# Kernel tuning notes

Measured on AMD Instinct MI355X. Metric: run time of the kernel, lower is better.

## Reference

```python
import jax, jax.numpy as jnp
import numpy as np

EMBED_DIM = 1024
Q_IN = 1024
KV_IN = 256
NUM_HEADS = 16
HEAD_DIM = EMBED_DIM // NUM_HEADS
SCALING = HEAD_DIM ** -0.5
BSZ, TGT, SRC = 8, 1024, 1024


def setup_inputs() -> dict:
    key = jax.random.key(0)
    ks = jax.random.split(key, 12)
    s = lambda fan_in: 1.0 / np.sqrt(fan_in)
    return {
        "hidden_states": jax.random.normal(ks[0], (BSZ, TGT, Q_IN), jnp.float32),
        "key_value_states": jax.random.normal(ks[1], (BSZ, SRC, KV_IN), jnp.float32),
        "attention_mask": jnp.zeros((BSZ, 1, TGT, SRC), jnp.float32),
        "layer_head_mask": jnp.ones((NUM_HEADS,), jnp.float32),
        "Wq": jax.random.normal(ks[2], (Q_IN, EMBED_DIM), jnp.float32) * s(Q_IN),
        "bq": jax.random.normal(ks[3], (EMBED_DIM,), jnp.float32) * 0.02,
        "Wk": jax.random.normal(ks[4], (KV_IN, EMBED_DIM), jnp.float32) * s(KV_IN),
        "bk": jax.random.normal(ks[5], (EMBED_DIM,), jnp.float32) * 0.02,
        "Wv": jax.random.normal(ks[6], (KV_IN, EMBED_DIM), jnp.float32) * s(KV_IN),
        "bv": jax.random.normal(ks[7], (EMBED_DIM,), jnp.float32) * 0.02,
        "Wo": jax.random.normal(ks[8], (EMBED_DIM, EMBED_DIM), jnp.float32) * s(EMBED_DIM),
        "bo": jax.random.normal(ks[9], (EMBED_DIM,), jnp.float32) * 0.02,
    }


def reference(hidden_states, key_value_states, attention_mask, layer_head_mask,
              Wq, bq, Wk, bk, Wv, bv, Wo, bo):
    b, t, _ = hidden_states.shape
    src = key_value_states.shape[1]
    # projections, split heads: [b, h, len, d]
    q = (hidden_states @ Wq + bq) * SCALING
    q = q.reshape(b, t, NUM_HEADS, HEAD_DIM).transpose(0, 2, 1, 3)
    k = (key_value_states @ Wk + bk).reshape(b, src, NUM_HEADS, HEAD_DIM).transpose(0, 2, 1, 3)
    v = (key_value_states @ Wv + bv).reshape(b, src, NUM_HEADS, HEAD_DIM).transpose(0, 2, 1, 3)
    # scores [b, h, t, src] + additive mask
    scores = jnp.einsum("bhtd,bhsd->bhts", q, k) + attention_mask
    probs = jax.nn.softmax(scores, axis=-1)
    # head mask multiply (dropout p=0 in eval)
    probs = probs * layer_head_mask[None, :, None, None]
    out = jnp.einsum("bhts,bhsd->bhtd", probs, v)
    out = out.transpose(0, 2, 1, 3).reshape(b, t, EMBED_DIM)
    return out @ Wo + bo
```

## Files before the change

### kernel.cpp

```cpp
#include <hip/hip_runtime.h>
#include <hip/hip_bf16.h>
#include <cstdint>

#define B_    8
#define T_    1024
#define S_    1024
#define E_    1024
#define NH_   16
#define HD_   64
#define KVIN_ 256
#define SCALE_ 0.125f

typedef __attribute__((ext_vector_type(8))) short bf16x8;
typedef __attribute__((ext_vector_type(4))) float f32x4;
typedef unsigned short us;

__device__ __forceinline__ us f2bf(float x) {
  union { float f; unsigned u; } v; v.f = x;
  unsigned r = v.u + 0x7fffu + ((v.u >> 16) & 1u);
  return (us)(r >> 16);
}

__device__ __forceinline__ us f2bf_p(float x) {
  union { float f; unsigned u; } v; v.f = x;
  return (us)((v.u + 0x8000u) >> 16);
}

__device__ __forceinline__ void gl_lds16(const us* g, const us* l) {
  __builtin_amdgcn_global_load_lds(
      (const __attribute__((address_space(1))) void*)g,
      (__attribute__((address_space(3))) void*)l, 16, 0, 0);
}

__device__ __forceinline__ void cvt_body8(const float* __restrict__ in,
                                          us* __restrict__ out, int blk, int tid) {
  #pragma unroll
  for (int j = 0; j < 8; ++j) {
    int i = blk * 2048 + j * 256 + tid;
    float4 v = ((const float4*)in)[i];
    ushort4 o;
    o.x = f2bf(v.x); o.y = f2bf(v.y); o.z = f2bf(v.z); o.w = f2bf(v.w);
    ((ushort4*)out)[i] = o;
  }
}

__device__ __forceinline__ void tr_body(const float* __restrict__ W,
                                        us* __restrict__ Wt,
                                        int K, int N, int bx, int by, int tid) {
  __shared__ float t[32][33];
  int n0 = bx * 32, k0 = by * 32;
  int tx = tid & 31, ty = tid >> 5;
  #pragma unroll
  for (int r = 0; r < 32; r += 8)
    t[ty + r][tx] = W[(size_t)(k0 + ty + r) * N + n0 + tx];
  __syncthreads();
  #pragma unroll
  for (int r = 0; r < 32; r += 8)
    Wt[(size_t)(n0 + ty + r) * K + k0 + tx] = f2bf(t[tx][ty + r]);
}

__global__ __launch_bounds__(256) void k_prep(const float* __restrict__ hs, us* __restrict__ hsb,
                                              const float* __restrict__ kv, us* __restrict__ kvb,
                                              const float* __restrict__ Wq, us* __restrict__ Wqt,
                                              const float* __restrict__ Wk, us* __restrict__ Wkt,
                                              const float* __restrict__ Wv, us* __restrict__ Wvt,
                                              const float* __restrict__ Wo, us* __restrict__ Wot) {
  const int bid = blockIdx.x, tid = threadIdx.x;
  if (bid < 1024) { cvt_body8(hs, hsb, bid, tid); return; }
  if (bid < 1280) { cvt_body8(kv, kvb, bid - 1024, tid); return; }
  int id = bid - 1280;
  if (id < 1024)      tr_body(Wq, Wqt, 1024, 1024, id & 31, id >> 5, tid);
  else if (id < 1280) tr_body(Wk, Wkt, 256, 1024, (id - 1024) & 31, (id - 1024) >> 5, tid);
  else if (id < 1536) tr_body(Wv, Wvt, 256, 1024, (id - 1280) & 31, (id - 1280) >> 5, tid);
  else                tr_body(Wo, Wot, 1024, 1024, (id - 1536) & 31, (id - 1536) >> 5, tid);
}

template <int EPI>
__device__ __forceinline__ void gemm_body(const us* __restrict__ A, int lda,
                                          const us* __restrict__ Bt, int ldb,
                                          const float* __restrict__ bias,
                                          void* __restrict__ Cv, int K) {
  __shared__ us smem[12288];
  us* As = smem;
  us* Bs = smem + 128 * 64;
  const int tid = threadIdx.x, lane = tid & 63, w = tid >> 6;
  const int quad = lane >> 4, lc = lane & 15;
  const int m0 = blockIdx.x * 128, n0 = blockIdx.y * 64;
  const int wm = (w >> 1) * 64, wn = (w & 1) * 32;

  f32x4 acc[4][2] = {};

  const int strow = lane >> 3;
  const int stcol = (((lane & 7) ^ ((lane >> 3) & 7)) * 8);
  const us* Ag = A + (size_t)(m0 + w * 32 + strow) * lda + stcol;
  const us* Bg = Bt + (size_t)(n0 + w * 16 + strow) * ldb + stcol;

  for (int k0 = 0; k0 < K; k0 += 64) {
    __syncthreads();
    #pragma unroll
    for (int r = 0; r < 4; ++r)
      gl_lds16(Ag + (size_t)r * 8 * lda + k0, As + (w * 4 + r) * 512);
    #pragma unroll
    for (int r = 0; r < 2; ++r)
      gl_lds16(Bg + (size_t)r * 8 * ldb + k0, Bs + (w * 2 + r) * 512);
    __syncthreads();
    #pragma unroll
    for (int ks = 0; ks < 2; ++ks) {
      bf16x8 af[4], bfr[2];
      #pragma unroll
      for (int i = 0; i < 4; ++i)
        af[i]  = *(const bf16x8*)(As + (wm + i * 16 + lc) * 64 + (((ks * 4 + quad) ^ (lc & 7)) * 8));
      #pragma unroll
      for (int i = 0; i < 2; ++i)
        bfr[i] = *(const bf16x8*)(Bs + (wn + i * 16 + lc) * 64 + (((ks * 4 + quad) ^ (lc & 7)) * 8));
      #pragma unroll
      for (int mt = 0; mt < 4; ++mt)
        #pragma unroll
        for (int nt = 0; nt < 2; ++nt)
          acc[mt][nt] = __builtin_amdgcn_mfma_f32_16x16x32_bf16(af[mt], bfr[nt], acc[mt][nt], 0, 0, 0);
    }
  }

  if constexpr (EPI == 2) {
    __syncthreads();
    #pragma unroll
    for (int nt = 0; nt < 2; ++nt) {
      const float bn = bias[n0 + wn + nt * 16 + lc];
      #pragma unroll
      for (int mt = 0; mt < 4; ++mt)
        #pragma unroll
        for (int r = 0; r < 4; ++r)
          smem[(wn + nt * 16 + lc) * 136 + wm + mt * 16 + quad * 4 + r] =
              f2bf(acc[mt][nt][r] + bn);
    }
    __syncthreads();
    const int nl = tid >> 2, sp = (tid & 3) * 32;
    const int bb = m0 >> 10, sw = m0 & 1023;
    us* dst = (us*)Cv + ((size_t)(bb * 1024) + n0 + nl) * 1024 + sw + sp;
    #pragma unroll
    for (int j = 0; j < 4; ++j) {
      uint4 v = *(const uint4*)(smem + nl * 136 + sp + j * 8);
      *(uint4*)(dst + j * 8) = v;
    }
    return;
  }

  #pragma unroll
  for (int mt = 0; mt < 4; ++mt) {
    #pragma unroll
    for (int nt = 0; nt < 2; ++nt) {
      const int n = n0 + wn + nt * 16 + lc;
      const float bn = bias[n];
      #pragma unroll
      for (int r = 0; r < 4; ++r) {
        const int m = m0 + wm + mt * 16 + quad * 4 + r;
        float v = acc[mt][nt][r] + bn;
        if constexpr (EPI == 0)
          ((us*)Cv)[(size_t)m * E_ + n] = f2bf(v * SCALE_);
        else if constexpr (EPI == 1)
          ((us*)Cv)[(size_t)m * E_ + n] = f2bf(v);
        else
          ((float*)Cv)[(size_t)m * E_ + n] = v;
      }
    }
  }
}

__global__ __launch_bounds__(256) void k_proj(const us* __restrict__ hsb,
                                              const us* __restrict__ kvb,
                                              const us* __restrict__ Wqt,
                                              const us* __restrict__ Wkt,
                                              const us* __restrict__ Wvt,
                                              const float* __restrict__ bq,
                                              const float* __restrict__ bk,
                                              const float* __restrict__ bv,
                                              us* __restrict__ Qb,
                                              us* __restrict__ Kb,
                                              us* __restrict__ Vtb) {
  const int z = blockIdx.z;
  if (z == 0)      gemm_body<0>(hsb, 1024, Wqt, 1024, bq, (void*)Qb, 1024);
  else if (z == 1) gemm_body<1>(kvb, 256, Wkt, 256, bk, (void*)Kb, 256);
  else             gemm_body<2>(kvb, 256, Wvt, 256, bv, (void*)Vtb, 256);
}

__global__ __launch_bounds__(256) void k_oproj(const us* __restrict__ Ob,
                                               const us* __restrict__ Wot,
                                               const float* __restrict__ bo,
                                               float* __restrict__ out) {
  gemm_body<3>(Ob, 1024, Wot, 1024, bo, (void*)out, 1024);
}

__global__ __launch_bounds__(256, 4) void k_attn(const us* __restrict__ Q,
                                                 const us* __restrict__ Kg_,
                                                 const us* __restrict__ Vt,
                                                 const float* __restrict__ mask,
                                                 const float* __restrict__ lhm,
                                                 us* __restrict__ O) {
  __shared__ us Ks[64 * 64];
  __shared__ us Vs[64 * 64];
  __shared__ us Ps[4][32 * 72];

  const int tid = threadIdx.x, lane = tid & 63, w = tid >> 6;
  const int quad = lane >> 4, lc = lane & 15;
  const int bidx = blockIdx.x;
  const int qt = bidx & 7;
  const int h = (bidx >> 3) & 15;
  const int b = bidx >> 7;
  const int q0 = qt * 128 + w * 32;

  bf16x8 qf[2][2];
  #pragma unroll
  for (int mt = 0; mt < 2; ++mt) {
    const us* Qrow = Q + ((size_t)(b * 1024 + q0 + mt * 16 + lc)) * 1024 + h * 64 + quad * 8;
    qf[mt][0] = *(const bf16x8*)Qrow;
    qf[mt][1] = *(const bf16x8*)(Qrow + 32);
  }

  f32x4 oacc[2][4] = {};
  f32x4 lacc[2] = {};

  bf16x8 ones;
  #pragma unroll
  for (int i = 0; i < 8; ++i) ones[i] = (short)0x3F80;

  const int stsw = (((lane & 7) ^ ((lane >> 3) & 7)) * 8);
  const us* Kgs = Kg_ + ((size_t)(b * 1024) + w * 16 + (lane >> 3)) * 1024 + h * 64 + stsw;
  const us* Vgs = Vt + ((size_t)((b * 16 + h) * 64) + w * 16 + (lane >> 3)) * 1024 + stsw;
  const float* mg = mask + ((size_t)(b * 1024 + q0 + quad * 4)) * 1024 + lc;

  for (int s0 = 0; s0 < 1024; s0 += 64) {
    __syncthreads();
    #pragma unroll
    for (int r = 0; r < 2; ++r) {
      gl_lds16(Kgs + (size_t)(s0 + r * 8) * 1024, Ks + (w * 16 + r * 8) * 64);
      gl_lds16(Vgs + (size_t)(r * 8) * 1024 + s0, Vs + (w * 16 + r * 8) * 64);
    }
    __syncthreads();

    #pragma unroll
    for (int mt = 0; mt < 2; ++mt) {
      float mv[4][4];
      #pragma unroll
      for (int nt = 0; nt < 4; ++nt)
        #pragma unroll
        for (int r = 0; r < 4; ++r)
          mv[nt][r] = mg[(size_t)(mt * 16 + r) * 1024 + s0 + nt * 16];

      f32x4 sacc[4] = {};
      #pragma unroll
      for (int ks = 0; ks < 2; ++ks)
        #pragma unroll
        for (int nt = 0; nt < 4; ++nt) {
          bf16x8 kf = *(const bf16x8*)(Ks + (nt * 16 + lc) * 64 + (((ks * 4 + quad) ^ (lc & 7)) * 8));
          sacc[nt] = __builtin_amdgcn_mfma_f32_16x16x32_bf16(qf[mt][ks], kf, sacc[nt], 0, 0, 0);
        }

      #pragma unroll
      for (int nt = 0; nt < 4; ++nt)
        #pragma unroll
        for (int r = 0; r < 4; ++r) {
          float pv = __expf(sacc[nt][r] + mv[nt][r]);
          Ps[w][(mt * 16 + quad * 4 + r) * 72 + nt * 16 + lc] = f2bf_p(pv);
        }
    }

    #pragma unroll
    for (int ks = 0; ks < 2; ++ks) {
      bf16x8 pf0 = *(const bf16x8*)(&Ps[w][(0  + lc) * 72 + ks * 32 + quad * 8]);
      bf16x8 pf1 = *(const bf16x8*)(&Ps[w][(16 + lc) * 72 + ks * 32 + quad * 8]);
      lacc[0] = __builtin_amdgcn_mfma_f32_16x16x32_bf16(pf0, ones, lacc[0], 0, 0, 0);
      lacc[1] = __builtin_amdgcn_mfma_f32_16x16x32_bf16(pf1, ones, lacc[1], 0, 0, 0);
      #pragma unroll
      for (int nt = 0; nt < 4; ++nt) {
        bf16x8 vf = *(const bf16x8*)(Vs + (nt * 16 + lc) * 64 + (((ks * 4 + quad) ^ (lc & 7)) * 8));
        oacc[0][nt] = __builtin_amdgcn_mfma_f32_16x16x32_bf16(pf0, vf, oacc[0][nt], 0, 0, 0);
        oacc[1][nt] = __builtin_amdgcn_mfma_f32_16x16x32_bf16(pf1, vf, oacc[1][nt], 0, 0, 0);
      }
    }
  }

  const float hm = lhm[h];
  #pragma unroll
  for (int mt = 0; mt < 2; ++mt) {
    us* Og = O + ((size_t)(b * 1024 + q0 + mt * 16 + quad * 4)) * 1024 + h * 64 + lc;
    #pragma unroll
    for (int r = 0; r < 4; ++r) {
      float inv = hm / lacc[mt][r];
      #pragma unroll
      for (int nt = 0; nt < 4; ++nt)
        Og[(size_t)r * 1024 + nt * 16] = f2bf(oacc[mt][nt][r] * inv);
    }
  }
}

extern "C" void kernel_launch(void* const* d_in, const int* in_sizes, int n_in,
                              void* d_out, int out_size, void* d_ws, size_t ws_size,
                              hipStream_t stream) {
  (void)in_sizes; (void)n_in; (void)out_size; (void)ws_size;
  const float* hs   = (const float*)d_in[0];
  const float* kv   = (const float*)d_in[1];
  const float* mask = (const float*)d_in[2];
  const float* lhm  = (const float*)d_in[3];
  const float* Wq   = (const float*)d_in[4];
  const float* bq   = (const float*)d_in[5];
  const float* Wk   = (const float*)d_in[6];
  const float* bk   = (const float*)d_in[7];
  const float* Wv   = (const float*)d_in[8];
  const float* bv   = (const float*)d_in[9];
  const float* Wo   = (const float*)d_in[10];
  const float* bo   = (const float*)d_in[11];
  float* out = (float*)d_out;

  char* p = (char*)d_ws;
  auto alloc = [&](size_t bytes) { char* r = p; p += (bytes + 255) & ~(size_t)255; return r; };
  us* hsb = (us*)alloc((size_t)B_ * T_ * E_ * 2);
  us* kvb = (us*)alloc((size_t)B_ * S_ * KVIN_ * 2);
  us* Wqt = (us*)alloc((size_t)E_ * E_ * 2);
  us* Wkt = (us*)alloc((size_t)E_ * KVIN_ * 2);
  us* Wvt = (us*)alloc((size_t)E_ * KVIN_ * 2);
  us* Wot = (us*)alloc((size_t)E_ * E_ * 2);
  us* Qb  = (us*)alloc((size_t)B_ * T_ * E_ * 2);
  us* Kb  = (us*)alloc((size_t)B_ * S_ * E_ * 2);
  us* Vtb = (us*)alloc((size_t)B_ * S_ * E_ * 2);
  us* Ob  = (us*)alloc((size_t)B_ * T_ * E_ * 2);

  k_prep<<<3840, 256, 0, stream>>>(hs, hsb, kv, kvb, Wq, Wqt, Wk, Wkt, Wv, Wvt, Wo, Wot);

  k_proj<<<dim3(64, 16, 3), 256, 0, stream>>>(hsb, kvb, Wqt, Wkt, Wvt, bq, bk, bv, Qb, Kb, Vtb);

  k_attn<<<1024, 256, 0, stream>>>(Qb, Kb, Vtb, mask, lhm, Ob);

  k_oproj<<<dim3(64, 16), 256, 0, stream>>>(Ob, Wot, bo, out);
}
```

Measured before the change: 265.8 us.

## Fuse Q projection into attention kernel and seed scores with mask

Computes each block's 128x64 Q tile directly inside the attention kernel with an MFMA GEMM over hidden_states and Wq, then stages it through LDS into fragments. The Q intermediate buffer and the Q branch of the projection launch are removed. This saves the Q write and re-read in global memory, at the cost of a serial 1024-deep K loop at attention start with no overlap. It also initialises the score accumulators with the mask values instead of adding them after the MFMA. LDS is merged into one shared array so the Q staging can reuse it.

```diff
diff --git a/kernel.cpp b/kernel.cpp
--- a/kernel.cpp
+++ b/kernel.cpp
@@ -155,9 +155,7 @@
       for (int r = 0; r < 4; ++r) {
         const int m = m0 + wm + mt * 16 + quad * 4 + r;
         float v = acc[mt][nt][r] + bn;
-        if constexpr (EPI == 0)
-          ((us*)Cv)[(size_t)m * E_ + n] = f2bf(v * SCALE_);
-        else if constexpr (EPI == 1)
+        if constexpr (EPI == 1)
           ((us*)Cv)[(size_t)m * E_ + n] = f2bf(v);
         else
           ((float*)Cv)[(size_t)m * E_ + n] = v;
@@ -166,21 +164,15 @@
   }
 }
 
-__global__ __launch_bounds__(256) void k_proj(const us* __restrict__ hsb,
-                                              const us* __restrict__ kvb,
-                                              const us* __restrict__ Wqt,
+__global__ __launch_bounds__(256) void k_proj(const us* __restrict__ kvb,
                                               const us* __restrict__ Wkt,
                                               const us* __restrict__ Wvt,
-                                              const float* __restrict__ bq,
                                               const float* __restrict__ bk,
                                               const float* __restrict__ bv,
-                                              us* __restrict__ Qb,
                                               us* __restrict__ Kb,
                                               us* __restrict__ Vtb) {
-  const int z = blockIdx.z;
-  if (z == 0)      gemm_body<0>(hsb, 1024, Wqt, 1024, bq, (void*)Qb, 1024);
-  else if (z == 1) gemm_body<1>(kvb, 256, Wkt, 256, bk, (void*)Kb, 256);
-  else             gemm_body<2>(kvb, 256, Wvt, 256, bv, (void*)Vtb, 256);
+  if (blockIdx.z == 0) gemm_body<1>(kvb, 256, Wkt, 256, bk, (void*)Kb, 256);
+  else                 gemm_body<2>(kvb, 256, Wvt, 256, bv, (void*)Vtb, 256);
 }
 
 __global__ __launch_bounds__(256) void k_oproj(const us* __restrict__ Ob,
@@ -190,15 +182,18 @@
   gemm_body<3>(Ob, 1024, Wot, 1024, bo, (void*)out, 1024);
 }
 
-__global__ __launch_bounds__(256, 4) void k_attn(const us* __restrict__ Q,
+__global__ __launch_bounds__(256, 4) void k_attn(const us* __restrict__ hsb,
+                                                 const us* __restrict__ Wqt,
+                                                 const float* __restrict__ bq,
                                                  const us* __restrict__ Kg_,
                                                  const us* __restrict__ Vt,
                                                  const float* __restrict__ mask,
                                                  const float* __restrict__ lhm,
                                                  us* __restrict__ O) {
-  __shared__ us Ks[64 * 64];
-  __shared__ us Vs[64 * 64];
-  __shared__ us Ps[4][32 * 72];
+  __shared__ us smem[17408];
+  us* Ks = smem;
+  us* Vs = smem + 4096;
+  us* Ps = smem + 8192;
 
   const int tid = threadIdx.x, lane = tid & 63, w = tid >> 6;
   const int quad = lane >> 4, lc = lane & 15;
@@ -208,12 +203,56 @@
   const int b = bidx >> 7;
   const int q0 = qt * 128 + w * 32;
 
+  const int strow = lane >> 3;
+  const int stcol = (((lane & 7) ^ ((lane >> 3) & 7)) * 8);
+
   bf16x8 qf[2][2];
-  #pragma unroll
-  for (int mt = 0; mt < 2; ++mt) {
-    const us* Qrow = Q + ((size_t)(b * 1024 + q0 + mt * 16 + lc)) * 1024 + h * 64 + quad * 8;
-    qf[mt][0] = *(const bf16x8*)Qrow;
-    qf[mt][1] = *(const bf16x8*)(Qrow + 32);
+  {
+    const us* Ag = hsb + (size_t)(b * 1024 + qt * 128 + w * 32 + strow) * 1024 + stcol;
+    const us* Bg = Wqt + (size_t)(h * 64 + w * 16 + strow) * 1024 + stcol;
+    f32x4 qacc[2][4] = {};
+    for (int k0 = 0; k0 < 1024; k0 += 64) {
+      __syncthreads();
+      #pragma unroll
+      for (int r = 0; r < 4; ++r)
+        gl_lds16(Ag + (size_t)r * 8 * 1024 + k0, smem + (w * 4 + r) * 512);
+      #pragma unroll
+      for (int r = 0; r < 2; ++r)
+        gl_lds16(Bg + (size_t)r * 8 * 1024 + k0, smem + 8192 + (w * 2 + r) * 512);
+      __syncthreads();
+      #pragma unroll
+      for (int ks = 0; ks < 2; ++ks) {
+        bf16x8 af[2], bfr[4];
+        #pragma unroll
+        for (int i = 0; i < 2; ++i)
+          af[i] = *(const bf16x8*)(smem + (w * 32 + i * 16 + lc) * 64 + (((ks * 4 + quad) ^ (lc & 7)) * 8));
+        #pragma unroll
+        for (int i = 0; i < 4; ++i)
+          bfr[i] = *(const bf16x8*)(smem + 8192 + (i * 16 + lc) * 64 + (((ks * 4 + quad) ^ (lc & 7)) * 8));
+        #pragma unroll
+        for (int mt = 0; mt < 2; ++mt)
+          #pragma unroll
+          for (int nt = 0; nt < 4; ++nt)
+            qacc[mt][nt] = __builtin_amdgcn_mfma_f32_16x16x32_bf16(af[mt], bfr[nt], qacc[mt][nt], 0, 0, 0);
+      }
+    }
+    __syncthreads();
+    #pragma unroll
+    for (int nt = 0; nt < 4; ++nt) {
+      const float bn = bq[h * 64 + nt * 16 + lc];
+      #pragma unroll
+      for (int mt = 0; mt < 2; ++mt)
+        #pragma unroll
+        for (int r = 0; r < 4; ++r)
+          Ps[w * 2304 + (mt * 16 + quad * 4 + r) * 72 + nt * 16 + lc] =
+              f2bf((qacc[mt][nt][r] + bn) * SCALE_);
+    }
+    __syncthreads();
+    #pragma unroll
+    for (int mt = 0; mt < 2; ++mt) {
+      qf[mt][0] = *(const bf16x8*)(&Ps[w * 2304 + (mt * 16 + lc) * 72 + quad * 8]);
+      qf[mt][1] = *(const bf16x8*)(&Ps[w * 2304 + (mt * 16 + lc) * 72 + 32 + quad * 8]);
+    }
   }
 
   f32x4 oacc[2][4] = {};
@@ -223,9 +262,8 @@
   #pragma unroll
   for (int i = 0; i < 8; ++i) ones[i] = (short)0x3F80;
 
-  const int stsw = (((lane & 7) ^ ((lane >> 3) & 7)) * 8);
-  const us* Kgs = Kg_ + ((size_t)(b * 1024) + w * 16 + (lane >> 3)) * 1024 + h * 64 + stsw;
-  const us* Vgs = Vt + ((size_t)((b * 16 + h) * 64) + w * 16 + (lane >> 3)) * 1024 + stsw;
+  const us* Kgs = Kg_ + ((size_t)(b * 1024) + w * 16 + strow) * 1024 + h * 64 + stcol;
+  const us* Vgs = Vt + ((size_t)((b * 16 + h) * 64) + w * 16 + strow) * 1024 + stcol;
   const float* mg = mask + ((size_t)(b * 1024 + q0 + quad * 4)) * 1024 + lc;
 
   for (int s0 = 0; s0 < 1024; s0 += 64) {
@@ -239,14 +277,13 @@
 
     #pragma unroll
     for (int mt = 0; mt < 2; ++mt) {
-      float mv[4][4];
+      f32x4 sacc[4];
       #pragma unroll
       for (int nt = 0; nt < 4; ++nt)
         #pragma unroll
         for (int r = 0; r < 4; ++r)
-          mv[nt][r] = mg[(size_t)(mt * 16 + r) * 1024 + s0 + nt * 16];
-
-      f32x4 sacc[4] = {};
+          sacc[nt][r] = mg[(size_t)(mt * 16 + r) * 1024 + s0 + nt * 16];
+
       #pragma unroll
       for (int ks = 0; ks < 2; ++ks)
         #pragma unroll
@@ -259,15 +296,15 @@
       for (int nt = 0; nt < 4; ++nt)
         #pragma unroll
         for (int r = 0; r < 4; ++r) {
-          float pv = __expf(sacc[nt][r] + mv[nt][r]);
-          Ps[w][(mt * 16 + quad * 4 + r) * 72 + nt * 16 + lc] = f2bf_p(pv);
+          float pv = __expf(sacc[nt][r]);
+          Ps[w * 2304 + (mt * 16 + quad * 4 + r) * 72 + nt * 16 + lc] = f2bf_p(pv);
         }
     }
 
     #pragma unroll
     for (int ks = 0; ks < 2; ++ks) {
-      bf16x8 pf0 = *(const bf16x8*)(&Ps[w][(0  + lc) * 72 + ks * 32 + quad * 8]);
-      bf16x8 pf1 = *(const bf16x8*)(&Ps[w][(16 + lc) * 72 + ks * 32 + quad * 8]);
+      bf16x8 pf0 = *(const bf16x8*)(&Ps[w * 2304 + (0  + lc) * 72 + ks * 32 + quad * 8]);
+      bf16x8 pf1 = *(const bf16x8*)(&Ps[w * 2304 + (16 + lc) * 72 + ks * 32 + quad * 8]);
       lacc[0] = __builtin_amdgcn_mfma_f32_16x16x32_bf16(pf0, ones, lacc[0], 0, 0, 0);
       lacc[1] = __builtin_amdgcn_mfma_f32_16x16x32_bf16(pf1, ones, lacc[1], 0, 0, 0);
       #pragma unroll
@@ -319,16 +356,15 @@
   us* Wkt = (us*)alloc((size_t)E_ * KVIN_ * 2);
   us* Wvt = (us*)alloc((size_t)E_ * KVIN_ * 2);
   us* Wot = (us*)alloc((size_t)E_ * E_ * 2);
-  us* Qb  = (us*)alloc((size_t)B_ * T_ * E_ * 2);
   us* Kb  = (us*)alloc((size_t)B_ * S_ * E_ * 2);
   us* Vtb = (us*)alloc((size_t)B_ * S_ * E_ * 2);
   us* Ob  = (us*)alloc((size_t)B_ * T_ * E_ * 2);
 
   k_prep<<<3840, 256, 0, stream>>>(hs, hsb, kv, kvb, Wq, Wqt, Wk, Wkt, Wv, Wvt, Wo, Wot);
 
-  k_proj<<<dim3(64, 16, 3), 256, 0, stream>>>(hsb, kvb, Wqt, Wkt, Wvt, bq, bk, bv, Qb, Kb, Vtb);
-
-  k_attn<<<1024, 256, 0, stream>>>(Qb, Kb, Vtb, mask, lhm, Ob);
+  k_proj<<<dim3(64, 16, 2), 256, 0, stream>>>(kvb, Wkt, Wvt, bk, bv, Kb, Vtb);
+
+  k_attn<<<1024, 256, 0, stream>>>(hsb, Wqt, bq, Kb, Vtb, mask, lhm, Ob);
 
   k_oproj<<<dim3(64, 16), 256, 0, stream>>>(Ob, Wot, bo, out);
 }
```

Result: no change. 264.0 us (-0.7%).
